# Optimization experiments

Measured on AMD Instinct MI355X. Metric: run time of the kernel, lower is better.

Reference implementation:

```python
import jax, jax.numpy as jnp
import numpy as np

PD = 3                      # spatial feature dim (z, y, x)
HB = 1024                   # hash base per lattice coordinate
HOFF = 512                  # offset: lattice coords assumed in [-512, 511]
FILL = np.int32(2**31 - 1)  # sentinel for padded hash slots
EPS = 2.220446049250313e-16 # np.finfo('float').eps as in the torch module

def _elev_mat():
    # Embedding onto hyperplane sum(x)=0 with std-dev scale factors
    # (canonical permutohedral-lattice elevation, Adams et al.).
    E = np.zeros((PD + 1, PD), np.float32)
    E[0] = 1.0
    for i in range(1, PD + 1):
        E[i, i - 1] = -i
        E[i, i:] = 1.0
    inv_std = np.sqrt(2.0 / 3.0) * (PD + 1)
    scale = inv_std / np.sqrt(np.arange(1, PD + 1) * np.arange(2, PD + 2))
    return (E * scale[None, :]).astype(np.float32)

_EMAT = _elev_mat()
_IU = np.triu(np.ones((PD + 1, PD + 1), bool), 1)   # j > i
_IL = np.tril(np.ones((PD + 1, PD + 1), bool), -1)  # j < i

def _hash(k):  # (..., PD) int32 -> (...,) int32, injective for |coord| < 512
    return ((k[..., 0] + HOFF) * HB + (k[..., 1] + HOFF)) * HB + (k[..., 2] + HOFF)

def permutohedral(values, features):
    """Splat-blur-slice Gaussian filter. values (N,VD), features (N,PD)."""
    N, VD = values.shape
    elevated = features @ jnp.asarray(_EMAT).T                  # (N, PD+1)
    # nearest remainder-0 lattice point (nearest multiple of PD+1, ties -> down)
    v = elevated / (PD + 1)
    up, down = jnp.ceil(v), jnp.floor(v)
    rem0 = jnp.where(up - v < v - down, up, down) * (PD + 1)
    diff = elevated - rem0
    lt = diff[:, :, None] < diff[:, None, :]
    le = diff[:, :, None] <= diff[:, None, :]
    rank = (lt & _IU).sum(-1) + (le & _IL).sum(-1)              # (N, PD+1) int32
    rank = rank + jnp.round(rem0.sum(-1) / (PD + 1)).astype(rank.dtype)[:, None]
    shift = jnp.where(rank < 0, PD + 1, 0) + jnp.where(rank > PD, -(PD + 1), 0)
    rank = rank + shift
    rem0 = rem0 + shift.astype(rem0.dtype)
    # barycentric coordinates inside the enclosing simplex
    t = (elevated - rem0) / (PD + 1)                            # (N, PD+1)
    ohA = jax.nn.one_hot(PD - rank, PD + 2, dtype=values.dtype)
    ohB = jax.nn.one_hot(PD + 1 - rank, PD + 2, dtype=values.dtype)
    b = (ohA * t[..., None]).sum(1) - (ohB * t[..., None]).sum(1)
    b = b.at[:, 0].add(1.0 + b[:, PD + 1])
    bary = b[:, :PD + 1]                                        # (N, PD+1)
    # keys of the PD+1 simplex vertices (first PD coords; last is implied)
    rem0i = rem0[:, :PD].astype(jnp.int32)
    ranki = rank[:, :PD].astype(jnp.int32)
    r = jnp.arange(PD + 1, dtype=jnp.int32)[None, :, None]
    keys = rem0i[:, None, :] + jnp.where(ranki[:, None, :] >= PD + 1 - r, r - (PD + 1), r)  # (N,PD+1,PD)
    h = _hash(keys).reshape(-1)                                 # (N*(PD+1),)
    M = h.shape[0]
    uh, inv = jnp.unique(h, size=M, fill_value=FILL, return_inverse=True)
    inv = inv.reshape(-1)
    # splat
    contrib = (values[:, None, :] * bary[:, :, None]).reshape(M, VD)
    lat = jax.ops.segment_sum(contrib, inv, num_segments=M)     # (M, VD)
    # decode unique keys from the (invertible) hash
    k2 = uh % HB - HOFF
    tq = uh // HB
    k1 = tq % HB - HOFF
    k0 = tq // HB - HOFF
    ukeys = jnp.stack([k0, k1, k2], -1).astype(jnp.int32)       # (M, PD)
    valid = (uh != FILL)[:, None]
    # blur with [0.5, 1, 0.5] along each of the PD+1 lattice directions
    def lookup(nk, lat_):
        nh = _hash(nk)
        idx = jnp.clip(jnp.searchsorted(uh, nh), 0, M - 1)
        ok = (uh[idx] == nh)[:, None]
        return jnp.where(ok, lat_[idx], 0.0)
    for j in range(PD + 1):
        o = np.ones(PD, np.int32)
        if j < PD:
            o[j] = -PD
        o = jnp.asarray(o)
        lat = jnp.where(valid, lat + 0.5 * (lookup(ukeys + o, lat) + lookup(ukeys - o, lat)), 0.0)
    # slice
    alpha = 1.0 / (1.0 + 2.0 ** (-PD))
    return alpha * jnp.einsum('nr,nrv->nv', bary, lat[inv.reshape(-1, PD + 1)])

def spatial_features(image, v_gamma, sigma_gamma):
    _, d, h, w = image.shape
    z = jnp.arange(d, dtype=jnp.float32)[:, None, None]
    y = jnp.arange(h, dtype=jnp.float32)[None, :, None]
    x = jnp.arange(w, dtype=jnp.float32)[None, None, :]
    zz = v_gamma[0] * jnp.broadcast_to(z, (d, h, w)) / sigma_gamma[0]
    xx = v_gamma[1] * jnp.broadcast_to(x, (d, h, w)) / sigma_gamma[1]
    yy = v_gamma[2] * jnp.broadcast_to(y, (d, h, w)) / sigma_gamma[2]
    return jnp.stack([zz, yy, xx], axis=3)                      # (d,h,w,3)

def setup_inputs() -> dict:
    key = jax.random.key(0)
    k1, k2 = jax.random.split(key)
    C, D, H, W = 4, 64, 128, 128
    return {
        'input_': jax.random.normal(k1, (C, D, H, W), jnp.float32),
        'image': jax.random.normal(k2, (1, D, H, W), jnp.float32),
        'v_gamma': jnp.ones((3,), jnp.float32),       # nn.Parameter init [1,1,1]
        'sigma_gamma': 5.0 * jnp.ones((3,), jnp.float32),
    }

def reference(input_, image, v_gamma, sigma_gamma):
    C, d, h, w = input_.shape
    N = d * h * w
    feats = spatial_features(image, v_gamma, sigma_gamma).reshape(N, PD)
    # filter q and the all-ones normalizer in one pass (linear per channel)
    vals = jnp.concatenate([input_.reshape(C, N).T, jnp.ones((N, 1), jnp.float32)], axis=1)
    out = permutohedral(vals, feats)
    q = out[:, :C].T.reshape(C, d, h, w)
    norm = out[:, C].reshape(1, d, h, w)
    return q * (1.0 / (norm + EPS))
```

## Files before the change

### kernel.cpp

```cpp
#include <hip/hip_runtime.h>


#define DD    64
#define HHH   128
#define WWW   128
#define NPTS  (DD * HHH * WWW)
#define LATN  (1 << 17)
#define LATF  (LATN * 5)
#define DQ    7
#define CELLS (DQ * DQ * DQ * 4)
#define MASKW ((CELLS + 31) / 32)

__device__ __forceinline__ int encK(int K0, int K1, int K2) {
    return ((K2 >> 2) << 12) | ((K1 >> 2) << 7) | ((K0 >> 2) << 2) | (K0 & 3);
}

__device__ __forceinline__ void pl_geom(int z, int y, int x,
                                        const float* __restrict__ vg,
                                        const float* __restrict__ sg,
                                        int* Kout , float* bout) {
    float f0 = vg[0] * (float)z / sg[0];
    float f1 = vg[2] * (float)y / sg[2];
    float f2 = vg[1] * (float)x / sg[1];

    const float m00 = (float)2.3094010767585034;
    const float m01 = (float)1.3333333333333333;
    const float m02 = (float)0.9428090415820634;
    const float m21 = (float)-2.6666666666666665;
    const float m32 = (float)-2.8284271247461903;

    float e[4];
    e[0] =  m00 * f0 + m01 * f1 + m02 * f2;
    e[1] = -m00 * f0 + m01 * f1 + m02 * f2;
    e[2] =  m21 * f1 + m02 * f2;
    e[3] =  m32 * f2;

    float rem0[4];
    int sumr = 0;
    #pragma unroll
    for (int i = 0; i < 4; ++i) {
        float v = e[i] * 0.25f;
        float up = ceilf(v), dn = floorf(v);
        float rr = ((up - v) < (v - dn)) ? up : dn;
        rem0[i] = rr * 4.0f;
        sumr += (int)rem0[i];
    }
    sumr /= 4;

    float diff[4];
    #pragma unroll
    for (int i = 0; i < 4; ++i) diff[i] = e[i] - rem0[i];
    int rank[4] = {0, 0, 0, 0};
    #pragma unroll
    for (int i = 0; i < 4; ++i)
        #pragma unroll
        for (int j = i + 1; j < 4; ++j) {
            if (diff[i] < diff[j]) rank[i]++; else rank[j]++;
        }

    #pragma unroll
    for (int i = 0; i < 4; ++i) {
        rank[i] += sumr;
        if (rank[i] < 0)      { rank[i] += 4; rem0[i] += 4.0f; }
        else if (rank[i] > 3) { rank[i] -= 4; rem0[i] -= 4.0f; }
    }

    float b[5] = {0.f, 0.f, 0.f, 0.f, 0.f};
    #pragma unroll
    for (int i = 0; i < 4; ++i) {
        float t = (e[i] - rem0[i]) * 0.25f;
        b[3 - rank[i]] += t;
        b[4 - rank[i]] -= t;
    }
    b[0] += 1.0f + b[4];

    int k0 = (int)rem0[0] + 16, k1 = (int)rem0[1] + 48, k2 = (int)rem0[2] + 88;
    #pragma unroll
    for (int r = 0; r < 4; ++r) {
        int o0 = (rank[0] >= 4 - r) ? (r - 4) : r;
        int o1 = (rank[1] >= 4 - r) ? (r - 4) : r;
        int o2 = (rank[2] >= 4 - r) ? (r - 4) : r;
        Kout[r * 3 + 0] = k0 + o0;
        Kout[r * 3 + 1] = k1 + o1;
        Kout[r * 3 + 2] = k2 + o2;
        bout[r] = b[r];
    }
}

__device__ __forceinline__ void pl_claim(int key, unsigned int* __restrict__ exists,
                                         int* __restrict__ wcnt, int* __restrict__ wl) {
    if (atomicExch(&exists[key], 1u) == 0u) {
        int p = atomicAdd(wcnt, 1);
        wl[p] = key;
    }
}

__device__ __forceinline__ int make_id(const int* K, int B0, int B1, int B2) {
    int l0 = K[0] - B0, l1 = K[1] - B1, l2 = K[2] - B2;
    if (((unsigned)l0 < 4u * DQ) & ((unsigned)l1 < 4u * DQ) & ((unsigned)l2 < 4u * DQ))
        return ((((l2 >> 2) * DQ) + (l1 >> 2)) * DQ + (l0 >> 2)) * 4 + (l0 & 3);
    return ~encK(K[0] & 127, K[1] & 127, K[2] & 127);
}

__device__ __forceinline__ void pl_emit(int id, const float* a,
                                        float* sacc, unsigned int* smask,
                                        float* __restrict__ mycopy,
                                        unsigned int* __restrict__ exists,
                                        int* __restrict__ wcnt, int* __restrict__ wl) {
    if (id >= 0) {
        #pragma unroll
        for (int c = 0; c < 5; ++c) atomicAdd(&sacc[id * 5 + c], a[c]);
        atomicOr(&smask[id >> 5], 1u << (id & 31));
    } else {
        int key = ~id;
        float* L = mycopy + (size_t)key * 5;
        #pragma unroll
        for (int c = 0; c < 5; ++c) atomicAdd(L + c, a[c]);
        pl_claim(key, exists, wcnt, wl);
    }
}

__global__ __launch_bounds__(256, 4)
void pl_splat(const float* __restrict__ vals, const float* __restrict__ vg,
              const float* __restrict__ sg, float* __restrict__ latc,
              unsigned int* __restrict__ exists,
              int* __restrict__ wcnt, int* __restrict__ wl) {
    __shared__ float sacc[CELLS * 5];
    __shared__ unsigned int smask[MASKW];
    for (int i = threadIdx.x; i < CELLS * 5; i += 256) sacc[i] = 0.f;
    for (int i = threadIdx.x; i < MASKW; i += 256) smask[i] = 0u;
    __syncthreads();

    int bt = blockIdx.x;
    int tx = (bt & 3) << 5;
    int ty = ((bt >> 2) & 15) << 3;
    int tz = (bt >> 6) << 2;

    float s0 = vg[0] / sg[0], s1 = vg[2] / sg[2], s2 = vg[1] / sg[1];
    const float m00 = 2.30940104f, m01 = 1.33333325f, m02 = 0.942809045f,
                m21 = -2.66666651f;
    float A0z = m00 * s0, A0y = m01 * s1, A0x = m02 * s2;
    float A1z = -A0z,     A1y = A0y,      A1x = A0x;
    float A2y = m21 * s1, A2x = A0x;
    float e0o = A0z * tz + A0y * ty + A0x * tx;
    float e1o = A1z * tz + A1y * ty + A1x * tx;
    float e2o = A2y * ty + A2x * tx;
    float e0m = e0o + fminf(0.f, A0z) * 3 + fminf(0.f, A0y) * 7 + fminf(0.f, A0x) * 31;
    float e1m = e1o + fminf(0.f, A1z) * 3 + fminf(0.f, A1y) * 7 + fminf(0.f, A1x) * 31;
    float e2m = e2o + fminf(0.f, A2y) * 7 + fminf(0.f, A2x) * 31;
    int B0 = ((int)floorf(e0m + 16.f - 7.f)) & ~3;
    int B1 = ((int)floorf(e1m + 48.f - 7.f)) & ~3;
    int B2 = ((int)floorf(e2m + 88.f - 7.f)) & ~3;

    int xs = threadIdx.x & 7;
    int xsl = ((xs & 3) << 1) | (xs >> 2);
    int x0 = tx + (xsl << 2);
    int y  = ty + ((threadIdx.x >> 3) & 7);
    int z  = tz + (threadIdx.x >> 6);
    int n0 = (z << 14) + (y << 7) + x0;

    float4 q0 = *(const float4*)(vals + n0);
    float4 q1 = *(const float4*)(vals + NPTS + n0);
    float4 q2 = *(const float4*)(vals + 2 * NPTS + n0);
    float4 q3 = *(const float4*)(vals + 3 * NPTS + n0);
    float ch0[4] = {q0.x, q0.y, q0.z, q0.w};
    float ch1[4] = {q1.x, q1.y, q1.z, q1.w};
    float ch2[4] = {q2.x, q2.y, q2.z, q2.w};
    float ch3[4] = {q3.x, q3.y, q3.z, q3.w};

    float* mycopy = latc + (size_t)(blockIdx.x & 3) * LATF;

    int cid[4];
    float acc[4][5];
    {
        int K[12]; float b[4];
        pl_geom(z, y, x0, vg, sg, K, b);
        #pragma unroll
        for (int r = 0; r < 4; ++r) {
            cid[r] = make_id(K + r * 3, B0, B1, B2);
            float w = b[r];
            acc[r][0] = w * ch0[0]; acc[r][1] = w * ch1[0];
            acc[r][2] = w * ch2[0]; acc[r][3] = w * ch3[0];
            acc[r][4] = w;
        }
    }
    #pragma unroll
    for (int p = 1; p < 4; ++p) {
        int K[12]; float b[4];
        pl_geom(z, y, x0 + p, vg, sg, K, b);
        #pragma unroll
        for (int r = 0; r < 4; ++r) {
            int id = make_id(K + r * 3, B0, B1, B2);
            float w = b[r];
            if (id == cid[r]) {
                acc[r][0] += w * ch0[p]; acc[r][1] += w * ch1[p];
                acc[r][2] += w * ch2[p]; acc[r][3] += w * ch3[p];
                acc[r][4] += w;
            } else {
                pl_emit(cid[r], acc[r], sacc, smask, mycopy, exists, wcnt, wl);
                cid[r] = id;
                acc[r][0] = w * ch0[p]; acc[r][1] = w * ch1[p];
                acc[r][2] = w * ch2[p]; acc[r][3] = w * ch3[p];
                acc[r][4] = w;
            }
        }
    }
    #pragma unroll
    for (int r = 0; r < 4; ++r)
        pl_emit(cid[r], acc[r], sacc, smask, mycopy, exists, wcnt, wl);

    __syncthreads();

    for (int i = threadIdx.x; i < CELLS; i += 256) {
        if (!((smask[i >> 5] >> (i & 31)) & 1u)) continue;
        int r = i & 3, q = i >> 2;
        int l0q = q % DQ; int t = q / DQ;
        int l1q = t % DQ; int l2q = t / DQ;
        int K0 = B0 + (l0q << 2) + r;
        int K1 = B1 + (l1q << 2) + r;
        int K2 = B2 + (l2q << 2) + r;
        int key = encK(K0 & 127, K1 & 127, K2 & 127);
        pl_claim(key, exists, wcnt, wl);
        float* L = mycopy + (size_t)key * 5;
        #pragma unroll
        for (int c = 0; c < 5; ++c) atomicAdd(L + c, sacc[i * 5 + c]);
    }
}

__global__ __launch_bounds__(256)
void pl_blur(const unsigned int* __restrict__ exists,
             const int* __restrict__ wl, const int* __restrict__ wcnt,
             const float* __restrict__ in, float* __restrict__ out,
             int d0, int d1, int d2, int first) {
    int total = (*wcnt) * 5;
    for (int i = blockIdx.x * 256 + threadIdx.x; i < total; i += 256 * 256) {
        int ci = i / 5, c = i - ci * 5;
        int didx = wl[ci];
        int r  = didx & 3;
        int K0 = (((didx >> 2)  & 31) << 2) | r;
        int K1 = (((didx >> 7)  & 31) << 2) | r;
        int K2 = (((didx >> 12) & 31) << 2) | r;
        size_t o = (size_t)didx * 5 + c;
        float ctr, n = 0.f;
        if (first)
            ctr = in[o] + in[LATF + o] + in[2 * LATF + o] + in[3 * LATF + o];
        else
            ctr = in[o];
        #pragma unroll
        for (int sgn = 0; sgn < 2; ++sgn) {
            int P0 = K0 + (sgn ? -d0 : d0);
            int P1 = K1 + (sgn ? -d1 : d1);
            int P2 = K2 + (sgn ? -d2 : d2);
            if (((unsigned)P0 < 128u) & ((unsigned)P1 < 128u) & ((unsigned)P2 < 128u)) {
                int nk = encK(P0, P1, P2);
                if (exists[nk]) {
                    size_t no = (size_t)nk * 5 + c;
                    if (first)
                        n += in[no] + in[LATF + no] + in[2 * LATF + no] + in[3 * LATF + no];
                    else
                        n += in[no];
                }
            }
        }
        out[o] = ctr + 0.5f * n;
    }
}

__global__ __launch_bounds__(256)
void pl_slice(const float* __restrict__ vg, const float* __restrict__ sg,
              const float* __restrict__ lat, float* __restrict__ out) {
    int n = blockIdx.x * 256 + threadIdx.x;
    if (n >= NPTS) return;
    int z = n >> 14;
    int y = (n >> 7) & 127;
    int x = n & 127;
    int K[12]; float b[4];
    pl_geom(z, y, x, vg, sg, K, b);
    float a0 = 0.f, a1 = 0.f, a2 = 0.f, a3 = 0.f, a4 = 0.f;
    #pragma unroll
    for (int r = 0; r < 4; ++r) {
        float w = b[r];
        int key = encK(K[r * 3] & 127, K[r * 3 + 1] & 127, K[r * 3 + 2] & 127);
        const float* L = lat + (size_t)key * 5;
        a0 += w * L[0]; a1 += w * L[1]; a2 += w * L[2]; a3 += w * L[3]; a4 += w * L[4];
    }
    const float alpha = (float)(1.0 / 1.125);
    float norm = alpha * a4 + (float)2.220446049250313e-16;
    float invn = 1.0f / norm;
    out[n]            = (alpha * a0) * invn;
    out[NPTS + n]     = (alpha * a1) * invn;
    out[2 * NPTS + n] = (alpha * a2) * invn;
    out[3 * NPTS + n] = (alpha * a3) * invn;
}

extern "C" void kernel_launch(void* const* d_in, const int* in_sizes, int n_in,
                              void* d_out, int out_size, void* d_ws, size_t ws_size,
                              hipStream_t stream) {
    const float* input = (const float*)d_in[0];
    const float* vg = (const float*)d_in[2];
    const float* sg = (const float*)d_in[3];
    float* out = (float*)d_out;

    char* ws = (char*)d_ws;
    float* latc = (float*)ws;
    unsigned int* exists = (unsigned int*)(latc + (size_t)4 * LATF);
    int* wcnt = (int*)(exists + LATN);
    int*   wl = (int*)(wcnt + 64);
    float* A  = (float*)(wl + LATN);
    float* B  = A + LATF;

    size_t zbytes = (size_t)4 * LATF * 4 + (size_t)LATN * 4 + 256;
    hipMemsetAsync(ws, 0, zbytes, stream);

    pl_splat<<<1024, dim3(256), 0, stream>>>(input, vg, sg, latc, exists, wcnt, wl);

    pl_blur<<<256, dim3(256), 0, stream>>>(exists, wl, wcnt, latc, A, -3, 1, 1, 1);
    pl_blur<<<256, dim3(256), 0, stream>>>(exists, wl, wcnt, A, B, 1, -3, 1, 0);
    pl_blur<<<256, dim3(256), 0, stream>>>(exists, wl, wcnt, B, A, 1, 1, -3, 0);
    pl_blur<<<256, dim3(256), 0, stream>>>(exists, wl, wcnt, A, B, 1, 1, 1, 0);

    pl_slice<<<NPTS / 256, dim3(256), 0, stream>>>(vg, sg, B, out);
}
```

Before: 154.7 us.

## Cut lattice copies to two, batch slice over four points, two-slot splat accumulator

```diff
diff --git a/kernel.cpp b/kernel.cpp
--- a/kernel.cpp
+++ b/kernel.cpp
@@ -7,18 +7,20 @@
 #define NPTS  (DD * HHH * WWW)
 #define LATN  (1 << 17)
 #define LATF  (LATN * 5)
+#define NCPY  2
 #define DQ    7
 #define CELLS (DQ * DQ * DQ * 4)
 #define MASKW ((CELLS + 31) / 32)
+#define NOID  0x7fffffff
 
 __device__ __forceinline__ int encK(int K0, int K1, int K2) {
     return ((K2 >> 2) << 12) | ((K1 >> 2) << 7) | ((K0 >> 2) << 2) | (K0 & 3);
 }
 
-__device__ __forceinline__ void pl_geom(int z, int y, int x,
-                                        const float* __restrict__ vg,
-                                        const float* __restrict__ sg,
-                                        int* Kout , float* bout) {
+__device__ __forceinline__ int pl_geom(int z, int y, int x,
+                                       const float* __restrict__ vg,
+                                       const float* __restrict__ sg,
+                                       int* Kout , float* bout) {
     float f0 = vg[0] * (float)z / sg[0];
     float f1 = vg[2] * (float)y / sg[2];
     float f2 = vg[1] * (float)x / sg[1];
@@ -39,10 +41,7 @@
     int sumr = 0;
     #pragma unroll
     for (int i = 0; i < 4; ++i) {
-        float v = e[i] * 0.25f;
-        float up = ceilf(v), dn = floorf(v);
-        float rr = ((up - v) < (v - dn)) ? up : dn;
-        rem0[i] = rr * 4.0f;
+        rem0[i] = rintf(e[i] * 0.25f) * 4.0f;
         sumr += (int)rem0[i];
     }
     sumr /= 4;
@@ -85,6 +84,8 @@
         Kout[r * 3 + 2] = k2 + o2;
         bout[r] = b[r];
     }
+    return ((k0 >> 2) + 32) | (((k1 >> 2) + 32) << 7) | (((k2 >> 2) + 32) << 14) |
+           (rank[0] << 21) | (rank[1] << 23) | (rank[2] << 25);
 }
 
 __device__ __forceinline__ void pl_claim(int key, unsigned int* __restrict__ exists,
@@ -125,10 +126,12 @@
               const float* __restrict__ sg, float* __restrict__ latc,
               unsigned int* __restrict__ exists,
               int* __restrict__ wcnt, int* __restrict__ wl) {
-    __shared__ float sacc[CELLS * 5];
+    __shared__ float4 sacc4[CELLS * 5 / 4 + 1];
     __shared__ unsigned int smask[MASKW];
-    for (int i = threadIdx.x; i < CELLS * 5; i += 256) sacc[i] = 0.f;
-    for (int i = threadIdx.x; i < MASKW; i += 256) smask[i] = 0u;
+    float* sacc = (float*)sacc4;
+    for (int i = threadIdx.x; i < CELLS * 5 / 4 + 1; i += 256)
+        sacc4[i] = make_float4(0.f, 0.f, 0.f, 0.f);
+    if (threadIdx.x < MASKW) smask[threadIdx.x] = 0u;
     __syncthreads();
 
     int bt = blockIdx.x;
@@ -168,20 +171,21 @@
     float ch2[4] = {q2.x, q2.y, q2.z, q2.w};
     float ch3[4] = {q3.x, q3.y, q3.z, q3.w};
 
-    float* mycopy = latc + (size_t)(blockIdx.x & 3) * LATF;
-
-    int cid[4];
-    float acc[4][5];
+    float* mycopy = latc + (size_t)(blockIdx.x & (NCPY - 1)) * LATF;
+
+    int cid[4], pid[4];
+    float cacc[4][5], pacc[4][5];
     {
         int K[12]; float b[4];
         pl_geom(z, y, x0, vg, sg, K, b);
         #pragma unroll
         for (int r = 0; r < 4; ++r) {
             cid[r] = make_id(K + r * 3, B0, B1, B2);
+            pid[r] = NOID;
             float w = b[r];
-            acc[r][0] = w * ch0[0]; acc[r][1] = w * ch1[0];
-            acc[r][2] = w * ch2[0]; acc[r][3] = w * ch3[0];
-            acc[r][4] = w;
+            cacc[r][0] = w * ch0[0]; cacc[r][1] = w * ch1[0];
+            cacc[r][2] = w * ch2[0]; cacc[r][3] = w * ch3[0];
+            cacc[r][4] = w;
         }
     }
     #pragma unroll
@@ -193,22 +197,28 @@
             int id = make_id(K + r * 3, B0, B1, B2);
             float w = b[r];
             if (id == cid[r]) {
-                acc[r][0] += w * ch0[p]; acc[r][1] += w * ch1[p];
-                acc[r][2] += w * ch2[p]; acc[r][3] += w * ch3[p];
-                acc[r][4] += w;
+                cacc[r][0] += w * ch0[p]; cacc[r][1] += w * ch1[p];
+                cacc[r][2] += w * ch2[p]; cacc[r][3] += w * ch3[p];
+                cacc[r][4] += w;
             } else {
-                pl_emit(cid[r], acc[r], sacc, smask, mycopy, exists, wcnt, wl);
+                if (pid[r] != NOID)
+                    pl_emit(pid[r], pacc[r], sacc, smask, mycopy, exists, wcnt, wl);
+                pid[r] = cid[r];
+                #pragma unroll
+                for (int c = 0; c < 5; ++c) pacc[r][c] = cacc[r][c];
                 cid[r] = id;
-                acc[r][0] = w * ch0[p]; acc[r][1] = w * ch1[p];
-                acc[r][2] = w * ch2[p]; acc[r][3] = w * ch3[p];
-                acc[r][4] = w;
+                cacc[r][0] = w * ch0[p]; cacc[r][1] = w * ch1[p];
+                cacc[r][2] = w * ch2[p]; cacc[r][3] = w * ch3[p];
+                cacc[r][4] = w;
             }
         }
     }
     #pragma unroll
-    for (int r = 0; r < 4; ++r)
-        pl_emit(cid[r], acc[r], sacc, smask, mycopy, exists, wcnt, wl);
-
+    for (int r = 0; r < 4; ++r) {
+        if (pid[r] != NOID)
+            pl_emit(pid[r], pacc[r], sacc, smask, mycopy, exists, wcnt, wl);
+        pl_emit(cid[r], cacc[r], sacc, smask, mycopy, exists, wcnt, wl);
+    }
     __syncthreads();
 
     for (int i = threadIdx.x; i < CELLS; i += 256) {
@@ -242,10 +252,8 @@
         int K2 = (((didx >> 12) & 31) << 2) | r;
         size_t o = (size_t)didx * 5 + c;
         float ctr, n = 0.f;
-        if (first)
-            ctr = in[o] + in[LATF + o] + in[2 * LATF + o] + in[3 * LATF + o];
-        else
-            ctr = in[o];
+        if (first) ctr = in[o] + in[LATF + o];
+        else       ctr = in[o];
         #pragma unroll
         for (int sgn = 0; sgn < 2; ++sgn) {
             int P0 = K0 + (sgn ? -d0 : d0);
@@ -255,10 +263,8 @@
                 int nk = encK(P0, P1, P2);
                 if (exists[nk]) {
                     size_t no = (size_t)nk * 5 + c;
-                    if (first)
-                        n += in[no] + in[LATF + no] + in[2 * LATF + no] + in[3 * LATF + no];
-                    else
-                        n += in[no];
+                    if (first) n += in[no] + in[LATF + no];
+                    else       n += in[no];
                 }
             }
         }
@@ -269,28 +275,46 @@
 __global__ __launch_bounds__(256)
 void pl_slice(const float* __restrict__ vg, const float* __restrict__ sg,
               const float* __restrict__ lat, float* __restrict__ out) {
-    int n = blockIdx.x * 256 + threadIdx.x;
-    if (n >= NPTS) return;
-    int z = n >> 14;
-    int y = (n >> 7) & 127;
-    int x = n & 127;
-    int K[12]; float b[4];
-    pl_geom(z, y, x, vg, sg, K, b);
-    float a0 = 0.f, a1 = 0.f, a2 = 0.f, a3 = 0.f, a4 = 0.f;
-    #pragma unroll
-    for (int r = 0; r < 4; ++r) {
-        float w = b[r];
-        int key = encK(K[r * 3] & 127, K[r * 3 + 1] & 127, K[r * 3 + 2] & 127);
-        const float* L = lat + (size_t)key * 5;
-        a0 += w * L[0]; a1 += w * L[1]; a2 += w * L[2]; a3 += w * L[3]; a4 += w * L[4];
-    }
-    const float alpha = (float)(1.0 / 1.125);
-    float norm = alpha * a4 + (float)2.220446049250313e-16;
-    float invn = 1.0f / norm;
-    out[n]            = (alpha * a0) * invn;
-    out[NPTS + n]     = (alpha * a1) * invn;
-    out[2 * NPTS + n] = (alpha * a2) * invn;
-    out[3 * NPTS + n] = (alpha * a3) * invn;
+    int t = blockIdx.x * 256 + threadIdx.x;
+    int n0 = t << 2;
+    int z = n0 >> 14;
+    int y = (n0 >> 7) & 127;
+    int x0 = n0 & 127;
+    float r0[4], r1[4], r2[4], r3[4];
+    int Sprev = -1;
+    float Lv[4][5];
+    #pragma unroll
+    for (int p = 0; p < 4; ++p) {
+        int K[12]; float b[4];
+        int S = pl_geom(z, y, x0 + p, vg, sg, K, b);
+        if (S != Sprev) {
+            Sprev = S;
+            #pragma unroll
+            for (int r = 0; r < 4; ++r) {
+                int key = encK(K[r * 3] & 127, K[r * 3 + 1] & 127, K[r * 3 + 2] & 127);
+                const float* L = lat + (size_t)key * 5;
+                #pragma unroll
+                for (int c = 0; c < 5; ++c) Lv[r][c] = L[c];
+            }
+        }
+        float a0 = 0.f, a1 = 0.f, a2 = 0.f, a3 = 0.f, a4 = 0.f;
+        #pragma unroll
+        for (int r = 0; r < 4; ++r) {
+            float w = b[r];
+            a0 += w * Lv[r][0]; a1 += w * Lv[r][1]; a2 += w * Lv[r][2];
+            a3 += w * Lv[r][3]; a4 += w * Lv[r][4];
+        }
+        const float alpha = (float)(1.0 / 1.125);
+        float invn = 1.0f / (alpha * a4 + (float)2.220446049250313e-16);
+        r0[p] = alpha * a0 * invn;
+        r1[p] = alpha * a1 * invn;
+        r2[p] = alpha * a2 * invn;
+        r3[p] = alpha * a3 * invn;
+    }
+    *(float4*)(out + n0)            = make_float4(r0[0], r0[1], r0[2], r0[3]);
+    *(float4*)(out + NPTS + n0)     = make_float4(r1[0], r1[1], r1[2], r1[3]);
+    *(float4*)(out + 2 * NPTS + n0) = make_float4(r2[0], r2[1], r2[2], r2[3]);
+    *(float4*)(out + 3 * NPTS + n0) = make_float4(r3[0], r3[1], r3[2], r3[3]);
 }
 
 extern "C" void kernel_launch(void* const* d_in, const int* in_sizes, int n_in,
@@ -303,13 +327,13 @@
 
     char* ws = (char*)d_ws;
     float* latc = (float*)ws;
-    unsigned int* exists = (unsigned int*)(latc + (size_t)4 * LATF);
+    unsigned int* exists = (unsigned int*)(latc + (size_t)NCPY * LATF);
     int* wcnt = (int*)(exists + LATN);
     int*   wl = (int*)(wcnt + 64);
     float* A  = (float*)(wl + LATN);
     float* B  = A + LATF;
 
-    size_t zbytes = (size_t)4 * LATF * 4 + (size_t)LATN * 4 + 256;
+    size_t zbytes = (size_t)NCPY * LATF * 4 + (size_t)LATN * 4 + 256;
     hipMemsetAsync(ws, 0, zbytes, stream);
 
     pl_splat<<<1024, dim3(256), 0, stream>>>(input, vg, sg, latc, exists, wcnt, wl);
@@ -319,5 +343,5 @@
     pl_blur<<<256, dim3(256), 0, stream>>>(exists, wl, wcnt, B, A, 1, 1, -3, 0);
     pl_blur<<<256, dim3(256), 0, stream>>>(exists, wl, wcnt, A, B, 1, 1, 1, 0);
 
-    pl_slice<<<NPTS / 256, dim3(256), 0, stream>>>(vg, sg, B, out);
-}
+    pl_slice<<<NPTS / 4 / 256, dim3(256), 0, stream>>>(vg, sg, B, out);
+}
```

Measured after the change: 154.0 us. No clear change (-0.5%).
